# Optimization experiments

Hardware: AMD Instinct MI355X
Metric: run time of the kernel (lower is better)

Reference implementation:

```python
import jax, jax.numpy as jnp
import numpy as np

EPS = 1e-12  # torch F.normalize eps


def _pairwise_sqdist(x, y):
    # P[b,i,j] = |x_i|^2 + |y_j|^2 - 2 x_i.y_j  (matches batch_pairwise_dist)
    rx = jnp.sum(x * x, axis=-1)[:, :, None]          # [B,N,1]
    ry = jnp.sum(y * y, axis=-1)[:, None, :]          # [B,1,M]
    zz = jnp.einsum('bnd,bmd->bnm', x, y)             # [B,N,M]
    return rx + ry - 2.0 * zz


def _unit_axis1(t):
    # torch F.normalize(t, dim=1): L2-normalize across the edge dimension (axis=1)
    n = jnp.sqrt(jnp.sum(t * t, axis=1, keepdims=True))
    return t / jnp.maximum(n, EPS)


def setup_inputs() -> dict:
    key = jax.random.key(0)
    k1, k2, k3, k4 = jax.random.split(key, 4)
    B, N, E = 2, 8192, 24576
    gts = jax.random.normal(k1, (B, N, 6), dtype=jnp.float32)
    preds = jax.random.normal(k2, (B, N, 6), dtype=jnp.float32)
    gts_normals = jax.random.normal(k3, (B, N, 3), dtype=jnp.float32)
    sphere_edges = jax.random.randint(k4, (E, 2), 0, N, dtype=jnp.int32)
    return {"gts": gts, "preds": preds, "gts_normals": gts_normals,
            "sphere_edges": sphere_edges}


def reference(gts, preds, gts_normals, sphere_edges):
    gts_points = gts[:, :, :3]
    preds_points = preds[:, :, :3]
    gts_colors = gts[:, :, 3:]
    preds_colors = preds[:, :, 3:]
    e0 = sphere_edges[:, 0]
    e1 = sphere_edges[:, 1]

    # ---- edge loss ----
    edge = preds_points[:, e0, :] - preds_points[:, e1, :]      # [B,E,3]
    edge_length = jnp.sum(jnp.abs(edge), axis=2)                # [B,E]
    edge_loss = jnp.sum(jnp.mean(edge_length, axis=1)) * 300.0

    # ---- color chamfer loss ----
    Pc = _pairwise_sqdist(gts_colors, preds_colors)             # [B,N,M]
    color_loss = jnp.sum(jnp.min(Pc, axis=1)) + jnp.sum(jnp.min(Pc, axis=2))

    # ---- point chamfer loss ----
    P = _pairwise_sqdist(gts_points, preds_points)              # [B,N,M]
    dist_f2s = jnp.min(P, axis=1)                               # [B,M]
    dist_s2f = jnp.min(P, axis=2)                               # [B,N]
    idx_s2f = jnp.argmin(P, axis=2)                             # [B,N] (into M)
    champfer_loss = (jnp.sum(jnp.mean(dist_f2s, axis=1))
                     + jnp.sum(jnp.mean(dist_s2f, axis=1)) * 0.55) * 3000.0

    # ---- normal loss ----
    # gather gts_normals by nearest-pred index (valid since N == M), then by edge start
    normal = jnp.take_along_axis(gts_normals, idx_s2f[:, :, None], axis=1)  # [B,N,3]
    normal = normal[:, e0, :]                                   # [B,E,3]
    # original casts edge to Long then back to float -> truncation toward zero
    edge_t = jnp.trunc(edge)
    cosine = jnp.abs(jnp.sum(_unit_axis1(normal) * _unit_axis1(edge_t), axis=2))
    normal_loss = jnp.sum(jnp.mean(cosine, axis=1)) * 0.5

    return color_loss + edge_loss + champfer_loss + normal_loss
```

## Files before the change

### kernel.cpp

```cpp
#include <hip/hip_runtime.h>
#include <stdint.h>

#define TPB 256
#define ROWS_PB 512
#define KROWS 8
#define TC 256
#define CS 16

typedef unsigned long long u64;
typedef unsigned int u32;

__device__ __forceinline__ float waveReduceSum(float v){
#pragma unroll
  for (int o = 32; o > 0; o >>= 1) v += __shfl_down(v, o, 64);
  return v;
}

__device__ __forceinline__ u32 aload_u32(u32* p){
  return __hip_atomic_load(p, __ATOMIC_ACQUIRE, __HIP_MEMORY_SCOPE_AGENT);
}
__device__ __forceinline__ float aload_f32(float* p){
  return __hip_atomic_load(p, __ATOMIC_ACQUIRE, __HIP_MEMORY_SCOPE_AGENT);
}

template<bool NEED_IDX>
__device__ __forceinline__ void pass_phase(
    const float* __restrict__ rows, const float* __restrict__ cols,
    u64* __restrict__ outPack, u32* __restrict__ outDist, u32* __restrict__ outCol,
    int N, int cpc, int b, int rb, int chunk,
    float4* ptsT, float4* colT, u64* mPack, u32* mCol)
{
  const int t = threadIdx.x, lane = t & 63, w = t >> 6;
  const int rowBase = rb * ROWS_PB, colBase = chunk * cpc;

  float ax[KROWS], ay[KROWS], az[KROWS], rx[KROWS];
  float cr[KROWS], cg_[KROWS], cb_[KROWS], rc[KROWS];
  float bD[KROWS], bC[KROWS];
  int bM[KROWS];
#pragma unroll
  for (int k = 0; k < KROWS; k++){
    const float* p = rows + ((size_t)b * N + (rowBase + lane + 64 * k)) * 6;
    float p0 = p[0], p1 = p[1], p2 = p[2], p3 = p[3], p4 = p[4], p5 = p[5];
    ax[k] = -2.f * p0; ay[k] = -2.f * p1; az[k] = -2.f * p2;
    rx[k] = fmaf(p0, p0, fmaf(p1, p1, p2 * p2));
    cr[k] = -2.f * p3; cg_[k] = -2.f * p4; cb_[k] = -2.f * p5;
    rc[k] = fmaf(p3, p3, fmaf(p4, p4, p5 * p5));
    bD[k] = 3.4e38f; bC[k] = 3.4e38f; bM[k] = 0;
  }
  mPack[t] = ~0ull; mPack[t + TPB] = ~0ull;
  mCol[t] = ~0u;    mCol[t + TPB] = ~0u;

  for (int tb = 0; tb < cpc; tb += TC){
    const float* p = cols + ((size_t)b * N + (colBase + tb + t)) * 6;
    float q0 = p[0], q1 = p[1], q2 = p[2], q3 = p[3], q4 = p[4], q5 = p[5];
    ptsT[t] = make_float4(q0, q1, q2, fmaf(q0, q0, fmaf(q1, q1, q2 * q2)));
    colT[t] = make_float4(q3, q4, q5, fmaf(q3, q3, fmaf(q4, q4, q5 * q5)));
    __syncthreads();
#pragma unroll 2
    for (int j = 0; j < TC / 4; j += 2){
      const int mlA = j * 4 + w, mlB = mlA + 4;
      const float4 pA = ptsT[mlA], pB = ptsT[mlB];
      const float4 cA = colT[mlA], cB = colT[mlB];
      const int gA = colBase + tb + mlA;
      const int gB = gA + 4;
#pragma unroll
      for (int k = 0; k < KROWS; k++){
        float tA = fmaf(ax[k], pA.x, fmaf(ay[k], pA.y, fmaf(az[k], pA.z, pA.w)));
        float tB = fmaf(ax[k], pB.x, fmaf(ay[k], pB.y, fmaf(az[k], pB.z, pB.w)));
        if (NEED_IDX){
          if (tA < bD[k]) { bD[k] = tA; bM[k] = gA; }
          if (tB < bD[k]) { bD[k] = tB; bM[k] = gB; }
        } else {
          bD[k] = fminf(fminf(tA, tB), bD[k]);
        }
        float eA = fmaf(cr[k], cA.x, fmaf(cg_[k], cA.y, fmaf(cb_[k], cA.z, cA.w)));
        float eB = fmaf(cr[k], cB.x, fmaf(cg_[k], cB.y, fmaf(cb_[k], cB.z, cB.w)));
        bC[k] = fminf(fminf(eA, eB), bC[k]);
      }
    }
    __syncthreads();
  }

#pragma unroll
  for (int k = 0; k < KROWS; k++){
    int r = lane + 64 * k;
    float dv = fmaxf(bD[k] + rx[k], 0.f);
    float cv = fmaxf(bC[k] + rc[k], 0.f);
    u64 pk = NEED_IDX ? (((u64)__float_as_uint(dv) << 32) | (u32)bM[k])
                      : ((u64)__float_as_uint(dv) << 32);
    atomicMin(&mPack[r], pk);
    atomicMin(&mCol[r], __float_as_uint(cv));
  }
  __syncthreads();
  for (int i = 0; i < ROWS_PB; i += TPB){
    int r = t + i;
    size_t g = (size_t)b * N + rowBase + r;
    if (NEED_IDX) atomicMin(&outPack[g], mPack[r]);
    else          atomicMin(&outDist[g], (u32)(mPack[r] >> 32));
    atomicMin(&outCol[g], mCol[r]);
  }
}

__global__ void __launch_bounds__(TPB) pass_kernel(
    const float* __restrict__ gts, const float* __restrict__ preds,
    u64* __restrict__ packS2F, u32* __restrict__ distF2S,
    u32* __restrict__ colMin2, u32* __restrict__ colMin1,
    int N, int cpc, int nPass)
{
  __shared__ __align__(16) char lds[14336];
  float4* ptsT = (float4*)lds;
  float4* colT = (float4*)(lds + 4096);
  u64* mPack   = (u64*)(lds + 8192);
  u32* mCol    = (u32*)(lds + 12288);

  const int x = (int)blockIdx.x;
  int perDB = nPass / 4;
  int dir = x / (2 * perDB);
  int rem = x - dir * 2 * perDB;
  int b = rem / perDB;
  int id = rem - b * perDB;
  int rb = id / CS, chunk = id - rb * CS;
  if (dir == 0) pass_phase<true >(gts,  preds, packS2F, distF2S, colMin2,
                                  N, cpc, b, rb, chunk, ptsT, colT, mPack, mCol);
  else          pass_phase<false>(preds, gts,  packS2F, distF2S, colMin1,
                                  N, cpc, b, rb, chunk, ptsT, colT, mPack, mCol);
}

__global__ void __launch_bounds__(TPB) finish_kernel(
    const float* __restrict__ preds, const float* __restrict__ normals,
    const int* __restrict__ edges,
    u64* __restrict__ packS2F, u32* __restrict__ distF2S,
    u32* __restrict__ colMin2, u32* __restrict__ colMin1,
    float* __restrict__ acc, float* __restrict__ out,
    int N, int E, int nRowBlk, int nEdgeBlk)
{
  __shared__ float rbuf[4];
  __shared__ float buf7[7][4];
  __shared__ float chn[3];

  u32* ctrEdge = (u32*)(acc + 15);
  u32* ctrFin  = (u32*)(acc + 16);
  const int x = (int)blockIdx.x;
  const int t = threadIdx.x;
  const int nTot = nRowBlk + nEdgeBlk;

  if (x < nRowBlk){
    int row = x * TPB + t;
    float invN = 1.f / (float)N;
    float s = 3000.f * invN * __uint_as_float(distF2S[row])
            + 1650.f * invN * __uint_as_float((u32)(packS2F[row] >> 32))
            + __uint_as_float(colMin1[row]) + __uint_as_float(colMin2[row]);
    s = waveReduceSum(s);
    if ((t & 63) == 0) rbuf[t >> 6] = s;
    __syncthreads();
    if (t == 0){
      atomicAdd(&acc[14], rbuf[0] + rbuf[1] + rbuf[2] + rbuf[3]);
      __threadfence();
      u32 old = atomicAdd(ctrFin, 1u);
      if (old == (u32)(nTot - 1)){
        float a0 = aload_f32(&acc[0]), a13 = aload_f32(&acc[13]), a14 = aload_f32(&acc[14]);
        out[0] = a14 + a0 * (300.f / (float)E) + a13 * (0.5f / (float)E);
      }
    }
    return;
  }

  int gid = (x - nRowBlk) * TPB + t;
  int b = gid / E, e = gid - b * E;
  int e0 = edges[2 * e], e1 = edges[2 * e + 1];
  const float* p0 = preds + ((size_t)b * N + e0) * 6;
  const float* p1 = preds + ((size_t)b * N + e1) * 6;
  float ex = p0[0] - p1[0], ey = p0[1] - p1[1], ez = p0[2] - p1[2];
  u32 idx = (u32)packS2F[(size_t)b * N + e0];
  const float* nr = normals + ((size_t)b * N + idx) * 3;
  float n0 = nr[0], n1 = nr[1], n2 = nr[2];
  float t0 = truncf(ex), t1 = truncf(ey), t2 = truncf(ez);
  {
    float v[7] = { fabsf(ex) + fabsf(ey) + fabsf(ez),
                   n0 * n0, n1 * n1, n2 * n2, t0 * t0, t1 * t1, t2 * t2 };
    int lane = t & 63, w = t >> 6;
#pragma unroll
    for (int q = 0; q < 7; q++){
      float s = waveReduceSum(v[q]);
      if (lane == 0) buf7[q][w] = s;
    }
    __syncthreads();
    if (t < 7){
      float s = buf7[t][0] + buf7[t][1] + buf7[t][2] + buf7[t][3];
      int off = (t == 0) ? 0 : ((t < 4) ? (1 + b * 3 + t - 1) : (7 + b * 3 + t - 4));
      atomicAdd(&acc[off], s);
    }
    __syncthreads();
    if (t == 0){ __threadfence(); atomicAdd(ctrEdge, 1u); }
  }
  if (t == 0){
    while (aload_u32(ctrEdge) < (u32)nEdgeBlk) __builtin_amdgcn_s_sleep(2);
#pragma unroll
    for (int c = 0; c < 3; c++){
      float Sn = aload_f32(&acc[1 + b * 3 + c]);
      float Se = aload_f32(&acc[7 + b * 3 + c]);
      chn[c] = 1.f / (fmaxf(sqrtf(Sn), 1e-12f) * fmaxf(sqrtf(Se), 1e-12f));
    }
  }
  __syncthreads();
  float cosv = fabsf(n0 * t0 * chn[0] + n1 * t1 * chn[1] + n2 * t2 * chn[2]);
  cosv = waveReduceSum(cosv);
  if ((t & 63) == 0) rbuf[t >> 6] = cosv;
  __syncthreads();
  if (t == 0){
    atomicAdd(&acc[13], rbuf[0] + rbuf[1] + rbuf[2] + rbuf[3]);
    __threadfence();
    u32 old = atomicAdd(ctrFin, 1u);
    if (old == (u32)(nTot - 1)){
      float a0 = aload_f32(&acc[0]), a13 = aload_f32(&acc[13]), a14 = aload_f32(&acc[14]);
      out[0] = a14 + a0 * (300.f / (float)E) + a13 * (0.5f / (float)E);
    }
  }
}

extern "C" void kernel_launch(void* const* d_in, const int* in_sizes, int n_in,
                              void* d_out, int out_size, void* d_ws, size_t ws_size,
                              hipStream_t stream)
{
  const float* gts     = (const float*)d_in[0];
  const float* preds   = (const float*)d_in[1];
  const float* normals = (const float*)d_in[2];
  const int*   edges   = (const int*)d_in[3];

  const int B = 2;
  const int BNtot = in_sizes[2] / 3;
  const int N = BNtot / B;
  const int E = in_sizes[3] / 2;

  char* ws = (char*)d_ws;
  float* acc   = (float*)ws;
  u64* packS2F = (u64*)(ws + 128);
  u32* distF2S = (u32*)(ws + 128 + (size_t)BNtot * 8);
  u32* colMin2 = (u32*)(ws + 128 + (size_t)BNtot * 12);
  u32* colMin1 = (u32*)(ws + 128 + (size_t)BNtot * 16);

  hipMemsetAsync(ws, 0, 128, stream);
  hipMemsetAsync(ws + 128, 0xFF, (size_t)BNtot * 20, stream);

  int cpc = N / CS;
  int nPass = 2 * B * (N / ROWS_PB) * CS;
  int nRowBlk = BNtot / TPB;
  int nEdgeBlk = (B * E) / TPB;

  pass_kernel<<<nPass, TPB, 0, stream>>>(gts, preds, packS2F, distF2S,
                                         colMin2, colMin1, N, cpc, nPass);
  finish_kernel<<<nRowBlk + nEdgeBlk, TPB, 0, stream>>>(
      preds, normals, edges, packS2F, distF2S, colMin2, colMin1,
      acc, (float*)d_out, N, E, nRowBlk, nEdgeBlk);
}
```

Before: 131.9 us.

## Compute both chamfer directions in one pass with index packed into float mantissa

Replaces the two-direction pass (gts→preds with index, preds→gts without) by a single pass over the distance matrix that reduces along rows in registers and along columns via wave shuffles plus LDS atomics. The argmin index is packed into the low 13 mantissa bits of the distance so a plain fminf replaces the compare-and-select. Column data is read straight from global memory with vector loads instead of being staged in LDS. This halves the pairwise distance work and shrinks workspace to 32-bit packs. In exchange the min distances are slightly truncated, tie-breaking changes, and the 13-bit index mask assumes N is at most 8192.

```diff
diff --git a/kernel.cpp b/kernel.cpp
--- a/kernel.cpp
+++ b/kernel.cpp
@@ -2,10 +2,10 @@
 #include <stdint.h>
 
 #define TPB 256
-#define ROWS_PB 512
-#define KROWS 8
-#define TC 256
+#define ROWS_PB 256
+#define KR 8
 #define CS 16
+#define IDXM 0x1FFFu
 
 typedef unsigned long long u64;
 typedef unsigned int u32;
@@ -23,113 +23,111 @@
   return __hip_atomic_load(p, __ATOMIC_ACQUIRE, __HIP_MEMORY_SCOPE_AGENT);
 }
 
-template<bool NEED_IDX>
-__device__ __forceinline__ void pass_phase(
-    const float* __restrict__ rows, const float* __restrict__ cols,
-    u64* __restrict__ outPack, u32* __restrict__ outDist, u32* __restrict__ outCol,
-    int N, int cpc, int b, int rb, int chunk,
-    float4* ptsT, float4* colT, u64* mPack, u32* mCol)
+__global__ void __launch_bounds__(TPB) pass_kernel(
+    const float* __restrict__ gts, const float* __restrict__ preds,
+    u32* __restrict__ packS2F, u32* __restrict__ distF2S,
+    u32* __restrict__ colMin2, u32* __restrict__ colMin1,
+    int N, int cpc)
 {
-  const int t = threadIdx.x, lane = t & 63, w = t >> 6;
-  const int rowBase = rb * ROWS_PB, colBase = chunk * cpc;
-
-  float ax[KROWS], ay[KROWS], az[KROWS], rx[KROWS];
-  float cr[KROWS], cg_[KROWS], cb_[KROWS], rc[KROWS];
-  float bD[KROWS], bC[KROWS];
-  int bM[KROWS];
-#pragma unroll
-  for (int k = 0; k < KROWS; k++){
-    const float* p = rows + ((size_t)b * N + (rowBase + lane + 64 * k)) * 6;
+  __shared__ u32 cminP[512];
+  __shared__ u32 cminC[512];
+
+  const int b = blockIdx.y;
+  const int rb = blockIdx.x / CS;
+  const int chunk = blockIdx.x - rb * CS;
+  const int t = threadIdx.x;
+  const int lane = t & 63, w = t >> 6;
+  const int ri = lane & 7, ci = lane >> 3;
+  const int rowBase = rb * ROWS_PB + w * 64 + ri * KR;
+  const int colBase = chunk * cpc;
+
+  for (int i = t; i < cpc; i += TPB){ cminP[i] = ~0u; cminC[i] = ~0u; }
+
+  float ax[KR], ay[KR], az[KR], rx[KR];
+  float cr[KR], cg_[KR], cb_[KR], rc[KR];
+  float bD[KR], bC[KR];
+#pragma unroll
+  for (int k = 0; k < KR; k++){
+    const float* p = gts + ((size_t)b * N + rowBase + k) * 6;
     float p0 = p[0], p1 = p[1], p2 = p[2], p3 = p[3], p4 = p[4], p5 = p[5];
     ax[k] = -2.f * p0; ay[k] = -2.f * p1; az[k] = -2.f * p2;
     rx[k] = fmaf(p0, p0, fmaf(p1, p1, p2 * p2));
     cr[k] = -2.f * p3; cg_[k] = -2.f * p4; cb_[k] = -2.f * p5;
     rc[k] = fmaf(p3, p3, fmaf(p4, p4, p5 * p5));
-    bD[k] = 3.4e38f; bC[k] = 3.4e38f; bM[k] = 0;
-  }
-  mPack[t] = ~0ull; mPack[t + TPB] = ~0ull;
-  mCol[t] = ~0u;    mCol[t + TPB] = ~0u;
-
-  for (int tb = 0; tb < cpc; tb += TC){
-    const float* p = cols + ((size_t)b * N + (colBase + tb + t)) * 6;
-    float q0 = p[0], q1 = p[1], q2 = p[2], q3 = p[3], q4 = p[4], q5 = p[5];
-    ptsT[t] = make_float4(q0, q1, q2, fmaf(q0, q0, fmaf(q1, q1, q2 * q2)));
-    colT[t] = make_float4(q3, q4, q5, fmaf(q3, q3, fmaf(q4, q4, q5 * q5)));
-    __syncthreads();
+    bD[k] = 3.4e38f; bC[k] = 3.4e38f;
+  }
+  __syncthreads();
+
+  const float* cbase = preds + ((size_t)b * N + colBase) * 6;
 #pragma unroll 2
-    for (int j = 0; j < TC / 4; j += 2){
-      const int mlA = j * 4 + w, mlB = mlA + 4;
-      const float4 pA = ptsT[mlA], pB = ptsT[mlB];
-      const float4 cA = colT[mlA], cB = colT[mlB];
-      const int gA = colBase + tb + mlA;
-      const int gB = gA + 4;
-#pragma unroll
-      for (int k = 0; k < KROWS; k++){
-        float tA = fmaf(ax[k], pA.x, fmaf(ay[k], pA.y, fmaf(az[k], pA.z, pA.w)));
-        float tB = fmaf(ax[k], pB.x, fmaf(ay[k], pB.y, fmaf(az[k], pB.z, pB.w)));
-        if (NEED_IDX){
-          if (tA < bD[k]) { bD[k] = tA; bM[k] = gA; }
-          if (tB < bD[k]) { bD[k] = tB; bM[k] = gB; }
-        } else {
-          bD[k] = fminf(fminf(tA, tB), bD[k]);
-        }
-        float eA = fmaf(cr[k], cA.x, fmaf(cg_[k], cA.y, fmaf(cb_[k], cA.z, cA.w)));
-        float eB = fmaf(cr[k], cB.x, fmaf(cg_[k], cB.y, fmaf(cb_[k], cB.z, cB.w)));
-        bC[k] = fminf(fminf(eA, eB), bC[k]);
-      }
-    }
-    __syncthreads();
-  }
-
-#pragma unroll
-  for (int k = 0; k < KROWS; k++){
-    int r = lane + 64 * k;
-    float dv = fmaxf(bD[k] + rx[k], 0.f);
-    float cv = fmaxf(bC[k] + rc[k], 0.f);
-    u64 pk = NEED_IDX ? (((u64)__float_as_uint(dv) << 32) | (u32)bM[k])
-                      : ((u64)__float_as_uint(dv) << 32);
-    atomicMin(&mPack[r], pk);
-    atomicMin(&mCol[r], __float_as_uint(cv));
-  }
-  __syncthreads();
-  for (int i = 0; i < ROWS_PB; i += TPB){
-    int r = t + i;
-    size_t g = (size_t)b * N + rowBase + r;
-    if (NEED_IDX) atomicMin(&outPack[g], mPack[r]);
-    else          atomicMin(&outDist[g], (u32)(mPack[r] >> 32));
-    atomicMin(&outCol[g], mCol[r]);
-  }
-}
-
-__global__ void __launch_bounds__(TPB) pass_kernel(
-    const float* __restrict__ gts, const float* __restrict__ preds,
-    u64* __restrict__ packS2F, u32* __restrict__ distF2S,
-    u32* __restrict__ colMin2, u32* __restrict__ colMin1,
-    int N, int cpc, int nPass)
-{
-  __shared__ __align__(16) char lds[14336];
-  float4* ptsT = (float4*)lds;
-  float4* colT = (float4*)(lds + 4096);
-  u64* mPack   = (u64*)(lds + 8192);
-  u32* mCol    = (u32*)(lds + 12288);
-
-  const int x = (int)blockIdx.x;
-  int perDB = nPass / 4;
-  int dir = x / (2 * perDB);
-  int rem = x - dir * 2 * perDB;
-  int b = rem / perDB;
-  int id = rem - b * perDB;
-  int rb = id / CS, chunk = id - rb * CS;
-  if (dir == 0) pass_phase<true >(gts,  preds, packS2F, distF2S, colMin2,
-                                  N, cpc, b, rb, chunk, ptsT, colT, mPack, mCol);
-  else          pass_phase<false>(preds, gts,  packS2F, distF2S, colMin1,
-                                  N, cpc, b, rb, chunk, ptsT, colT, mPack, mCol);
+  for (int j = 0; j < cpc / 16; j++){
+    const int c0 = j * 16 + ci * 2;
+    const float* qp = cbase + (size_t)c0 * 6;
+    const float4 qa  = *(const float4*)qp;
+    const float2 qb  = *(const float2*)(qp + 4);
+    const float2 r0  = *(const float2*)(qp + 6);
+    const float2 r1  = *(const float2*)(qp + 8);
+    const float2 r2  = *(const float2*)(qp + 10);
+    const float ryA = fmaf(qa.x, qa.x, fmaf(qa.y, qa.y, qa.z * qa.z));
+    const float rcA = fmaf(qa.w, qa.w, fmaf(qb.x, qb.x, qb.y * qb.y));
+    const float ryB = fmaf(r0.x, r0.x, fmaf(r0.y, r0.y, r1.x * r1.x));
+    const float rcB = fmaf(r1.y, r1.y, fmaf(r2.x, r2.x, r2.y * r2.y));
+    const u32 gA = (u32)(colBase + c0), gB = gA + 1;
+    float cpA = 3.4e38f, cpB = 3.4e38f, ccA = 3.4e38f, ccB = 3.4e38f;
+#pragma unroll
+    for (int k = 0; k < KR; k++){
+      float dA = fmaf(az[k], qa.z, fmaf(ay[k], qa.y, fmaf(ax[k], qa.x, ryA + rx[k])));
+      float dB = fmaf(az[k], r1.x, fmaf(ay[k], r0.y, fmaf(ax[k], r0.x, ryB + rx[k])));
+      float pkA = __uint_as_float((__float_as_uint(dA) & ~IDXM) | gA);
+      float pkB = __uint_as_float((__float_as_uint(dB) & ~IDXM) | gB);
+      bD[k] = fminf(fminf(pkA, pkB), bD[k]);
+      cpA = fminf(cpA, dA); cpB = fminf(cpB, dB);
+      float eA = fmaf(cb_[k], qb.y, fmaf(cg_[k], qb.x, fmaf(cr[k], qa.w, rcA + rc[k])));
+      float eB = fmaf(cb_[k], r2.y, fmaf(cg_[k], r2.x, fmaf(cr[k], r1.y, rcB + rc[k])));
+      bC[k] = fminf(fminf(eA, eB), bC[k]);
+      ccA = fminf(ccA, eA); ccB = fminf(ccB, eB);
+    }
+#pragma unroll
+    for (int m = 1; m < 8; m <<= 1){
+      cpA = fminf(cpA, __shfl_xor(cpA, m, 64));
+      cpB = fminf(cpB, __shfl_xor(cpB, m, 64));
+      ccA = fminf(ccA, __shfl_xor(ccA, m, 64));
+      ccB = fminf(ccB, __shfl_xor(ccB, m, 64));
+    }
+    if (ri == 0){
+      atomicMin(&cminP[c0],     __float_as_uint(cpA));
+      atomicMin(&cminP[c0 + 1], __float_as_uint(cpB));
+      atomicMin(&cminC[c0],     __float_as_uint(ccA));
+      atomicMin(&cminC[c0 + 1], __float_as_uint(ccB));
+    }
+  }
+
+#pragma unroll
+  for (int k = 0; k < KR; k++){
+    float d = bD[k], c = bC[k];
+#pragma unroll
+    for (int m = 8; m < 64; m <<= 1){
+      d = fminf(d, __shfl_xor(d, m, 64));
+      c = fminf(c, __shfl_xor(c, m, 64));
+    }
+    if (ci == 0){
+      size_t g = (size_t)b * N + rowBase + k;
+      atomicMin(&packS2F[g], __float_as_uint(d));
+      atomicMin(&colMin2[g], __float_as_uint(c));
+    }
+  }
+  __syncthreads();
+  for (int i = t; i < cpc; i += TPB){
+    size_t g = (size_t)b * N + colBase + i;
+    atomicMin(&distF2S[g], cminP[i]);
+    atomicMin(&colMin1[g], cminC[i]);
+  }
 }
 
 __global__ void __launch_bounds__(TPB) finish_kernel(
     const float* __restrict__ preds, const float* __restrict__ normals,
     const int* __restrict__ edges,
-    u64* __restrict__ packS2F, u32* __restrict__ distF2S,
+    u32* __restrict__ packS2F, u32* __restrict__ distF2S,
     u32* __restrict__ colMin2, u32* __restrict__ colMin1,
     float* __restrict__ acc, float* __restrict__ out,
     int N, int E, int nRowBlk, int nEdgeBlk)
@@ -147,8 +145,9 @@
   if (x < nRowBlk){
     int row = x * TPB + t;
     float invN = 1.f / (float)N;
+    float s2f = __uint_as_float(packS2F[row] & ~IDXM);
     float s = 3000.f * invN * __uint_as_float(distF2S[row])
-            + 1650.f * invN * __uint_as_float((u32)(packS2F[row] >> 32))
+            + 1650.f * invN * s2f
             + __uint_as_float(colMin1[row]) + __uint_as_float(colMin2[row]);
     s = waveReduceSum(s);
     if ((t & 63) == 0) rbuf[t >> 6] = s;
@@ -171,7 +170,7 @@
   const float* p0 = preds + ((size_t)b * N + e0) * 6;
   const float* p1 = preds + ((size_t)b * N + e1) * 6;
   float ex = p0[0] - p1[0], ey = p0[1] - p1[1], ez = p0[2] - p1[2];
-  u32 idx = (u32)packS2F[(size_t)b * N + e0];
+  u32 idx = packS2F[(size_t)b * N + e0] & IDXM;
   const float* nr = normals + ((size_t)b * N + idx) * 3;
   float n0 = nr[0], n1 = nr[1], n2 = nr[2];
   float t0 = truncf(ex), t1 = truncf(ey), t2 = truncf(ez);
@@ -234,21 +233,21 @@
 
   char* ws = (char*)d_ws;
   float* acc   = (float*)ws;
-  u64* packS2F = (u64*)(ws + 128);
-  u32* distF2S = (u32*)(ws + 128 + (size_t)BNtot * 8);
-  u32* colMin2 = (u32*)(ws + 128 + (size_t)BNtot * 12);
-  u32* colMin1 = (u32*)(ws + 128 + (size_t)BNtot * 16);
+  u32* packS2F = (u32*)(ws + 128);
+  u32* distF2S = (u32*)(ws + 128 + (size_t)BNtot * 4);
+  u32* colMin2 = (u32*)(ws + 128 + (size_t)BNtot * 8);
+  u32* colMin1 = (u32*)(ws + 128 + (size_t)BNtot * 12);
 
   hipMemsetAsync(ws, 0, 128, stream);
-  hipMemsetAsync(ws + 128, 0xFF, (size_t)BNtot * 20, stream);
+  hipMemsetAsync(ws + 128, 0xFF, (size_t)BNtot * 16, stream);
 
   int cpc = N / CS;
-  int nPass = 2 * B * (N / ROWS_PB) * CS;
+  dim3 gp((N / ROWS_PB) * CS, B);
+  pass_kernel<<<gp, TPB, 0, stream>>>(gts, preds, packS2F, distF2S,
+                                      colMin2, colMin1, N, cpc);
+
   int nRowBlk = BNtot / TPB;
   int nEdgeBlk = (B * E) / TPB;
-
-  pass_kernel<<<nPass, TPB, 0, stream>>>(gts, preds, packS2F, distF2S,
-                                         colMin2, colMin1, N, cpc, nPass);
   finish_kernel<<<nRowBlk + nEdgeBlk, TPB, 0, stream>>>(
       preds, normals, edges, packS2F, distF2S, colMin2, colMin1,
       acc, (float*)d_out, N, E, nRowBlk, nEdgeBlk);
```

New measurement: 153.4 us. 1.16x slower.
